# Performance work log

Measured on AMD Instinct MI355X. Metric: run time of the kernel, lower is better.

## Reference

```python
import jax, jax.numpy as jnp
import numpy as np

ALPHA = 0.25
GAMMA = 2.0
OBJ_POS_WEIGHT = 1.5
CLS_W, REG_W, OBJ_W = 2.5, 5.0, 0.5
B, M, C, IMG = 64, 50, 4, 1280


def setup_inputs() -> dict:
    key = jax.random.key(0)
    ks = jax.random.split(key, 12)
    shapes = {
        'cls_p3': (B, C, 160, 160), 'reg_p3': (B, 4, 160, 160), 'obj_p3': (B, 1, 160, 160),
        'cls_p4': (B, C, 80, 80),   'reg_p4': (B, 4, 80, 80),   'obj_p4': (B, 1, 80, 80),
        'cls_p5': (B, C, 40, 40),   'reg_p5': (B, 4, 40, 40),   'obj_p5': (B, 1, 40, 40),
    }
    inp = {name: jax.random.normal(k, s, dtype=jnp.float32)
           for (name, s), k in zip(shapes.items(), ks[:9])}
    # boxes in pixel xyxy: sample two corners uniformly, sort so x2>=x1, y2>=y1
    raw = jax.random.uniform(ks[9], (B, M, 4), dtype=jnp.float32) * IMG
    x1 = jnp.minimum(raw[..., 0], raw[..., 2]); x2 = jnp.maximum(raw[..., 0], raw[..., 2])
    y1 = jnp.minimum(raw[..., 1], raw[..., 3]); y2 = jnp.maximum(raw[..., 1], raw[..., 3])
    inp['boxes'] = jnp.stack([x1, y1, x2, y2], axis=-1)
    inp['labels'] = jax.random.randint(ks[10], (B, M), 0, C, dtype=jnp.int32)
    inp['box_valid'] = jax.random.randint(ks[11], (B, M), 0, 2, dtype=jnp.int32)
    inp['img_size'] = IMG
    return inp


def _bce_logits(x, t):
    # numerically stable BCE-with-logits, elementwise
    return jnp.maximum(x, 0.0) - x * t + jnp.log1p(jnp.exp(-jnp.abs(x)))


def _focal(x, t):
    bce = _bce_logits(x, t)
    p = jax.nn.sigmoid(x)
    p_t = p * t + (1.0 - p) * (1.0 - t)
    a_w = ALPHA * t + (1.0 - ALPHA) * (1.0 - t)
    return jnp.mean(a_w * (1.0 - p_t) ** GAMMA * bce)


def _smooth_l1(d):
    a = jnp.abs(d)
    return jnp.where(a < 1.0, 0.5 * d * d, a - 0.5)


def _build_targets(boxes, labels, valid, stride, Bn, Cn, H, W):
    cx = (boxes[..., 0] + boxes[..., 2]) * 0.5 / stride  # [B,M]
    cy = (boxes[..., 1] + boxes[..., 3]) * 0.5 / stride
    gx = jnp.clip(cx.astype(jnp.int32), 0, W - 1)
    gy = jnp.clip(cy.astype(jnp.int32), 0, H - 1)
    gy_s = jnp.where(valid > 0, gy, H)  # invalid boxes -> out of bounds -> dropped
    b = jnp.broadcast_to(jnp.arange(Bn)[:, None], gx.shape)
    w = jnp.maximum(boxes[..., 2] - boxes[..., 0], 1.0)
    h = jnp.maximum(boxes[..., 3] - boxes[..., 1], 1.0)
    vals = jnp.stack([cx - gx.astype(cx.dtype), cy - gy.astype(cy.dtype),
                      jnp.log(w / stride), jnp.log(h / stride)], axis=-1)  # [B,M,4]
    cls_t = jnp.zeros((Bn, Cn, H, W), jnp.float32).at[b, labels, gy_s, gx].set(1.0, mode='drop')
    obj_t = jnp.zeros((Bn, 1, H, W), jnp.float32).at[b, 0, gy_s, gx].set(1.0, mode='drop')
    ch = jnp.arange(4)
    reg_t = jnp.zeros((Bn, 4, H, W), jnp.float32).at[
        b[:, :, None], ch[None, None, :], gy_s[:, :, None], gx[:, :, None]].set(vals, mode='drop')
    mask = jnp.zeros((Bn, 1, H, W), jnp.float32).at[b, 0, gy_s, gx].set(1.0, mode='drop')
    return cls_t, reg_t, obj_t, mask


def _detection_loss(scales, boxes, labels, valid):
    total_cls = jnp.float32(0.0); total_reg = jnp.float32(0.0); total_obj = jnp.float32(0.0)
    for (cls_p, reg_p, obj_p, stride) in scales:
        Bn, Cn, H, W = cls_p.shape
        cls_t, reg_t, obj_t, mask = _build_targets(boxes, labels, valid, stride, Bn, Cn, H, W)
        total_cls = total_cls + _focal(cls_p, cls_t)
        # BCEWithLogits with pos_weight on positives, mean reduction
        obj_bce = -(OBJ_POS_WEIGHT * obj_t * jax.nn.log_sigmoid(obj_p)
                    + (1.0 - obj_t) * jax.nn.log_sigmoid(-obj_p))
        total_obj = total_obj + jnp.mean(obj_bce)
        mask4 = jnp.broadcast_to(mask, reg_p.shape)
        denom = jnp.sum(mask4)
        reg_l = jnp.sum(_smooth_l1(reg_p - reg_t) * mask4) / jnp.maximum(denom, 1.0)
        total_reg = total_reg + jnp.where(denom > 0, reg_l, 0.0)
    total = CLS_W * total_cls + REG_W * total_reg + OBJ_W * total_obj
    return total, total_cls, total_reg, total_obj


def reference(cls_p3, reg_p3, obj_p3, cls_p4, reg_p4, obj_p4, cls_p5, reg_p5, obj_p5,
              boxes, labels, box_valid, img_size):
    scales = [(cls_p3, reg_p3, obj_p3, 8.0),
              (cls_p4, reg_p4, obj_p4, 16.0),
              (cls_p5, reg_p5, obj_p5, 32.0)]
    return _detection_loss(scales, boxes, labels, box_valid)
```

## Files before the change

kernel.cpp:

```cpp
#include <hip/hip_runtime.h>
#include <math.h>

static constexpr int Bn = 64, Mn = 50, Cn = 4;
static constexpr int CORR_BLOCKS = 64;
static constexpr int DENSE_BLOCKS = 512;
static constexpr int TOTAL_BLOCKS = CORR_BLOCKS + DENSE_BLOCKS;

static constexpr int BASE_OFF = 12 * 64;

#define LOG2E 1.4426950408889634f
#define LN2   0.6931471805599453f

__device__ __forceinline__ float frcp (float x){ return __builtin_amdgcn_rcpf(x); }
__device__ __forceinline__ float fexp2(float x){ return __builtin_amdgcn_exp2f(x); }
__device__ __forceinline__ float flog2(float x){ return __builtin_amdgcn_logf(x); }

__device__ __forceinline__ float proc4(float4 v, float cf) {
  float s = 0.f;
  const float* px = &v.x;
#pragma unroll
  for (int k = 0; k < 4; ++k) {
    float x = px[k];
    float e   = fexp2(-LOG2E * fabsf(x));
    float ope = 1.f + e;
    float u   = frcp(ope);
    float sp  = fmaxf(x, 0.f) + LN2 * flog2(ope);
    float p   = (x >= 0.f) ? u : (1.f - u);
    float w   = fmaf(cf, fmaf(0.75f, p * p, -1.f), 1.f);
    s = fmaf(sp, w, s);
  }
  return s;
}

__device__ __forceinline__ float wave_reduce(float v) {
#pragma unroll
  for (int off = 32; off > 0; off >>= 1) v += __shfl_down(v, off, 64);
  return v;
}

__global__ __launch_bounds__(1024, 8) void main_kernel(
    const float* __restrict__ cls3, const float* __restrict__ reg3, const float* __restrict__ obj3,
    const float* __restrict__ cls4, const float* __restrict__ reg4, const float* __restrict__ obj4,
    const float* __restrict__ cls5, const float* __restrict__ reg5, const float* __restrict__ obj5,
    const float* __restrict__ boxes, const int* __restrict__ labels, const int* __restrict__ valid,
    float* __restrict__ ws) {
  if (blockIdx.x < CORR_BLOCKS) {
    __shared__ int s_cell[3][Mn];
    __shared__ int s_lab[Mn];
    __shared__ float cacc[12];

    const int b = blockIdx.x;
    const int tid = threadIdx.x;
    if (tid < 12) cacc[tid] = 0.f;

    const int s = tid / Mn;
    const int m = tid - s * Mn;

    float x1 = 0.f, y1 = 0.f, x2 = 0.f, y2 = 0.f;
    int lab = 0, val = 0;
    float cx = 0.f, cy = 0.f, strf = 8.f;
    int gx = 0, gy = 0, cell = -1, W = 160;

    if (tid < 150) {
      const float* bp = boxes + ((size_t)b * Mn + m) * 4;
      x1 = bp[0]; y1 = bp[1]; x2 = bp[2]; y2 = bp[3];
      lab = labels[b * Mn + m];
      val = valid[b * Mn + m];
      if (s == 0) s_lab[m] = lab;

      W = 160 >> s;
      strf = (float)(8 << s);
      if (val > 0) {
        float inv_s = frcp(strf);
        cx = (x1 + x2) * 0.5f * inv_s;
        cy = (y1 + y2) * 0.5f * inv_s;
        gx = min(max((int)cx, 0), W - 1);
        gy = min(max((int)cy, 0), W - 1);
        cell = gy * W + gx;
      }
      s_cell[s][m] = cell;
    }
    __syncthreads();

    if (tid < 150 && cell >= 0) {
      const float* clsP = (s == 0) ? cls3 : ((s == 1) ? cls4 : cls5);
      const float* regP = (s == 0) ? reg3 : ((s == 1) ? reg4 : reg5);
      const float* objP = (s == 0) ? obj3 : ((s == 1) ? obj4 : obj5);

      bool firstObj = true, lastReg = true, firstCls = true;
      for (int j = 0; j < Mn; ++j) {
        if (j == m) continue;
        if (s_cell[s][j] != cell) continue;
        if (j < m) {
          firstObj = false;
          if (s_lab[j] == lab) firstCls = false;
        } else {
          lastReg = false;
        }
      }
      size_t plane = (size_t)W * W;
      size_t pix = (size_t)gy * W + gx;

      if (firstObj) {
        float x = objP[(size_t)b * plane + pix];
        float e = fexp2(-LOG2E * fabsf(x));
        float sp = fmaxf(x, 0.f) + LN2 * flog2(1.f + e);
        float corr = 0.5f * sp - 1.5f * x;
        atomicAdd(&cacc[3 + s], corr);
        atomicAdd(&cacc[9 + s], 4.0f);
      }
      if (firstCls) {
        float x = clsP[((size_t)b * Cn + lab) * plane + pix];
        float e = fexp2(-LOG2E * fabsf(x));
        float ope = 1.f + e;
        float u = frcp(ope);
        float sp = fmaxf(x, 0.f) + LN2 * flog2(ope);
        float spn = sp - x;
        float p = (x >= 0.f) ? u : (1.f - u);
        float q = 1.f - p;
        float corr = 0.25f * q * q * spn - 0.75f * p * p * sp;
        atomicAdd(&cacc[0 + s], corr);
      }
      if (lastReg) {
        float w = fmaxf(x2 - x1, 1.f), h = fmaxf(y2 - y1, 1.f);
        float inv_s = frcp(strf);
        float t0 = cx - (float)gx, t1 = cy - (float)gy;
        float t2 = LN2 * flog2(w * inv_s), t3 = LN2 * flog2(h * inv_s);
        const float* rp = regP + (size_t)b * 4 * plane + pix;
        float sum = 0.f, d, a;
        d = rp[0]         - t0; a = fabsf(d); sum += (a < 1.f) ? 0.5f * d * d : a - 0.5f;
        d = rp[plane]     - t1; a = fabsf(d); sum += (a < 1.f) ? 0.5f * d * d : a - 0.5f;
        d = rp[2 * plane] - t2; a = fabsf(d); sum += (a < 1.f) ? 0.5f * d * d : a - 0.5f;
        d = rp[3 * plane] - t3; a = fabsf(d); sum += (a < 1.f) ? 0.5f * d * d : a - 0.5f;
        atomicAdd(&cacc[6 + s], sum);
      }
    }
    __syncthreads();
    if (tid < 12) ws[tid * 64 + b] = cacc[tid];
  } else {
    __shared__ float sdata[16];
    const int d = (int)blockIdx.x - CORR_BLOCKS;
    const int tid = threadIdx.x;

    const float4* sb; int bk, nB, nT; float cf;
    if (d < 311)      { sb = (const float4*)cls3; bk = d;       nB = 311; nT = 1600; cf = 1.f; }
    else if (d < 389) { sb = (const float4*)cls4; bk = d - 311; nB = 78;  nT = 400;  cf = 1.f; }
    else if (d < 409) { sb = (const float4*)cls5; bk = d - 389; nB = 20;  nT = 100;  cf = 1.f; }
    else if (d < 487) { sb = (const float4*)obj3; bk = d - 409; nB = 78;  nT = 400;  cf = 0.f; }
    else if (d < 507) { sb = (const float4*)obj4; bk = d - 487; nB = 20;  nT = 100;  cf = 0.f; }
    else              { sb = (const float4*)obj5; bk = d - 507; nB = 5;   nT = 25;   cf = 0.f; }

    float s = 0.f;
    int t = bk;
    float4 v = sb[(size_t)t * 1024 + tid];
    for (t += nB; t < nT; t += nB) {
      float4 vn = sb[(size_t)t * 1024 + tid];
      s += proc4(v, cf);
      v = vn;
    }
    s += proc4(v, cf);

    s = wave_reduce(s);
    const int lane = tid & 63;
    const int wid = tid >> 6;
    if (lane == 0) sdata[wid] = s;
    __syncthreads();
    if (tid == 0) {
      float r = 0.f;
#pragma unroll
      for (int i = 0; i < 16; ++i) r += sdata[i];
      ws[BASE_OFF + d] = r;
    }
  }
}

__global__ __launch_bounds__(256) void finalize_kernel(
    const float* __restrict__ ws, float* __restrict__ out) {
  __shared__ float sdata[6][4];
  __shared__ float res[18];
  const int t = threadIdx.x;
  const int lane = t & 63;
  const int wid = t >> 6;

  float a0 = 0.f, a1 = 0.f, a2 = 0.f, a3 = 0.f, a4 = 0.f, a5 = 0.f;
  for (int i = t; i < DENSE_BLOCKS; i += 256) {
    float v = ws[BASE_OFF + i];
    if (i < 311)      a0 += v;
    else if (i < 389) a1 += v;
    else if (i < 409) a2 += v;
    else if (i < 487) a3 += v;
    else if (i < 507) a4 += v;
    else              a5 += v;
  }
  float acc[6] = {a0, a1, a2, a3, a4, a5};
#pragma unroll
  for (int k = 0; k < 6; ++k) {
    float s = wave_reduce(acc[k]);
    if (lane == 0) sdata[k][wid] = s;
  }
  __syncthreads();
  if (t < 6) res[t] = sdata[t][0] + sdata[t][1] + sdata[t][2] + sdata[t][3];

  if (wid == 0) {
#pragma unroll
    for (int j = 0; j < 12; ++j) {
      float v = ws[j * 64 + lane];
      v = wave_reduce(v);
      if (lane == 0) res[6 + j] = v;
    }
  }
  __syncthreads();

  if (t == 0) {
    const float cls_cnt[3] = {6553600.f, 1638400.f, 409600.f};
    const float obj_cnt[3] = {1638400.f, 409600.f, 102400.f};
    float tc = 0.f, to = 0.f, tr = 0.f;
#pragma unroll
    for (int s = 0; s < 3; ++s) {
      tc += (res[s] + res[6 + s]) / cls_cnt[s];
      to += (res[3 + s] + res[9 + s]) / obj_cnt[s];
      float den = res[15 + s];
      if (den > 0.f) tr += res[12 + s] / fmaxf(den, 1.f);
    }
    float total = 2.5f * tc + 5.0f * tr + 0.5f * to;
    out[0] = total; out[1] = tc; out[2] = tr; out[3] = to;
  }
}

extern "C" void kernel_launch(void* const* d_in, const int* in_sizes, int n_in,
                              void* d_out, int out_size, void* d_ws, size_t ws_size,
                              hipStream_t stream) {
  const float* cls3 = (const float*)d_in[0];
  const float* reg3 = (const float*)d_in[1];
  const float* obj3 = (const float*)d_in[2];
  const float* cls4 = (const float*)d_in[3];
  const float* reg4 = (const float*)d_in[4];
  const float* obj4 = (const float*)d_in[5];
  const float* cls5 = (const float*)d_in[6];
  const float* reg5 = (const float*)d_in[7];
  const float* obj5 = (const float*)d_in[8];
  const float* boxes = (const float*)d_in[9];
  const int* labels = (const int*)d_in[10];
  const int* valid = (const int*)d_in[11];
  float* ws = (float*)d_ws;
  float* out = (float*)d_out;

  main_kernel<<<TOTAL_BLOCKS, 1024, 0, stream>>>(
      cls3, reg3, obj3, cls4, reg4, obj4, cls5, reg5, obj5,
      boxes, labels, valid, ws);

  finalize_kernel<<<1, 256, 0, stream>>>(ws, out);
}
```

Measured before the change: 22.94 us.

## Fuse correction work into dense blocks and issue fixed five-load chunks per block

The separate correction blocks are removed. Their box-matching work now runs inside the first 64 dense blocks, after those blocks have already issued their dense loads. Each dense block now handles exactly five float4 chunks per thread, loaded up front instead of through a strided loop, giving 525 evenly sized blocks. The goal is to hide load latency behind the correction work and to balance per-block load. The cost is higher register pressure and longer run times for the first 64 blocks.

```diff
diff --git a/kernel.cpp b/kernel.cpp
--- a/kernel.cpp
+++ b/kernel.cpp
@@ -2,9 +2,7 @@
 #include <math.h>
 
 static constexpr int Bn = 64, Mn = 50, Cn = 4;
-static constexpr int CORR_BLOCKS = 64;
-static constexpr int DENSE_BLOCKS = 512;
-static constexpr int TOTAL_BLOCKS = CORR_BLOCKS + DENSE_BLOCKS;
+static constexpr int TOTAL_BLOCKS = 525;
 
 static constexpr int BASE_OFF = 12 * 64;
 
@@ -44,13 +42,31 @@
     const float* __restrict__ cls5, const float* __restrict__ reg5, const float* __restrict__ obj5,
     const float* __restrict__ boxes, const int* __restrict__ labels, const int* __restrict__ valid,
     float* __restrict__ ws) {
-  if (blockIdx.x < CORR_BLOCKS) {
+  __shared__ float sdata[16];
+  const int bid = blockIdx.x;
+  const int tid = threadIdx.x;
+
+  const float4* sb; int lb; float cf;
+  if (bid < 320)      { sb = (const float4*)cls3; lb = bid;       cf = 1.f; }
+  else if (bid < 400) { sb = (const float4*)cls4; lb = bid - 320; cf = 1.f; }
+  else if (bid < 420) { sb = (const float4*)cls5; lb = bid - 400; cf = 1.f; }
+  else if (bid < 500) { sb = (const float4*)obj3; lb = bid - 420; cf = 0.f; }
+  else if (bid < 520) { sb = (const float4*)obj4; lb = bid - 500; cf = 0.f; }
+  else                { sb = (const float4*)obj5; lb = bid - 520; cf = 0.f; }
+
+  const float4* p = sb + (size_t)lb * 5120 + tid;
+  float4 v0 = p[0];
+  float4 v1 = p[1024];
+  float4 v2 = p[2048];
+  float4 v3 = p[3072];
+  float4 v4 = p[4096];
+
+  if (bid < 64) {
     __shared__ int s_cell[3][Mn];
     __shared__ int s_lab[Mn];
     __shared__ float cacc[12];
 
-    const int b = blockIdx.x;
-    const int tid = threadIdx.x;
+    const int b = bid;
     if (tid < 12) cacc[tid] = 0.f;
 
     const int s = tid / Mn;
@@ -116,9 +132,9 @@
         float u = frcp(ope);
         float sp = fmaxf(x, 0.f) + LN2 * flog2(ope);
         float spn = sp - x;
-        float p = (x >= 0.f) ? u : (1.f - u);
-        float q = 1.f - p;
-        float corr = 0.25f * q * q * spn - 0.75f * p * p * sp;
+        float p2 = (x >= 0.f) ? u : (1.f - u);
+        float q = 1.f - p2;
+        float corr = 0.25f * q * q * spn - 0.75f * p2 * p2 * sp;
         atomicAdd(&cacc[0 + s], corr);
       }
       if (lastReg) {
@@ -127,50 +143,31 @@
         float t0 = cx - (float)gx, t1 = cy - (float)gy;
         float t2 = LN2 * flog2(w * inv_s), t3 = LN2 * flog2(h * inv_s);
         const float* rp = regP + (size_t)b * 4 * plane + pix;
-        float sum = 0.f, d, a;
-        d = rp[0]         - t0; a = fabsf(d); sum += (a < 1.f) ? 0.5f * d * d : a - 0.5f;
-        d = rp[plane]     - t1; a = fabsf(d); sum += (a < 1.f) ? 0.5f * d * d : a - 0.5f;
-        d = rp[2 * plane] - t2; a = fabsf(d); sum += (a < 1.f) ? 0.5f * d * d : a - 0.5f;
-        d = rp[3 * plane] - t3; a = fabsf(d); sum += (a < 1.f) ? 0.5f * d * d : a - 0.5f;
+        float sum = 0.f, dd, a;
+        dd = rp[0]         - t0; a = fabsf(dd); sum += (a < 1.f) ? 0.5f * dd * dd : a - 0.5f;
+        dd = rp[plane]     - t1; a = fabsf(dd); sum += (a < 1.f) ? 0.5f * dd * dd : a - 0.5f;
+        dd = rp[2 * plane] - t2; a = fabsf(dd); sum += (a < 1.f) ? 0.5f * dd * dd : a - 0.5f;
+        dd = rp[3 * plane] - t3; a = fabsf(dd); sum += (a < 1.f) ? 0.5f * dd * dd : a - 0.5f;
         atomicAdd(&cacc[6 + s], sum);
       }
     }
     __syncthreads();
     if (tid < 12) ws[tid * 64 + b] = cacc[tid];
-  } else {
-    __shared__ float sdata[16];
-    const int d = (int)blockIdx.x - CORR_BLOCKS;
-    const int tid = threadIdx.x;
-
-    const float4* sb; int bk, nB, nT; float cf;
-    if (d < 311)      { sb = (const float4*)cls3; bk = d;       nB = 311; nT = 1600; cf = 1.f; }
-    else if (d < 389) { sb = (const float4*)cls4; bk = d - 311; nB = 78;  nT = 400;  cf = 1.f; }
-    else if (d < 409) { sb = (const float4*)cls5; bk = d - 389; nB = 20;  nT = 100;  cf = 1.f; }
-    else if (d < 487) { sb = (const float4*)obj3; bk = d - 409; nB = 78;  nT = 400;  cf = 0.f; }
-    else if (d < 507) { sb = (const float4*)obj4; bk = d - 487; nB = 20;  nT = 100;  cf = 0.f; }
-    else              { sb = (const float4*)obj5; bk = d - 507; nB = 5;   nT = 25;   cf = 0.f; }
-
-    float s = 0.f;
-    int t = bk;
-    float4 v = sb[(size_t)t * 1024 + tid];
-    for (t += nB; t < nT; t += nB) {
-      float4 vn = sb[(size_t)t * 1024 + tid];
-      s += proc4(v, cf);
-      v = vn;
-    }
-    s += proc4(v, cf);
-
-    s = wave_reduce(s);
-    const int lane = tid & 63;
-    const int wid = tid >> 6;
-    if (lane == 0) sdata[wid] = s;
-    __syncthreads();
-    if (tid == 0) {
-      float r = 0.f;
-#pragma unroll
-      for (int i = 0; i < 16; ++i) r += sdata[i];
-      ws[BASE_OFF + d] = r;
-    }
+  }
+
+  float s = proc4(v0, cf) + proc4(v1, cf) + proc4(v2, cf)
+          + proc4(v3, cf) + proc4(v4, cf);
+
+  s = wave_reduce(s);
+  const int lane = tid & 63;
+  const int wid = tid >> 6;
+  if (lane == 0) sdata[wid] = s;
+  __syncthreads();
+  if (tid == 0) {
+    float r = 0.f;
+#pragma unroll
+    for (int i = 0; i < 16; ++i) r += sdata[i];
+    ws[BASE_OFF + bid] = r;
   }
 }
 
@@ -183,13 +180,13 @@
   const int wid = t >> 6;
 
   float a0 = 0.f, a1 = 0.f, a2 = 0.f, a3 = 0.f, a4 = 0.f, a5 = 0.f;
-  for (int i = t; i < DENSE_BLOCKS; i += 256) {
+  for (int i = t; i < TOTAL_BLOCKS; i += 256) {
     float v = ws[BASE_OFF + i];
-    if (i < 311)      a0 += v;
-    else if (i < 389) a1 += v;
-    else if (i < 409) a2 += v;
-    else if (i < 487) a3 += v;
-    else if (i < 507) a4 += v;
+    if (i < 320)      a0 += v;
+    else if (i < 400) a1 += v;
+    else if (i < 420) a2 += v;
+    else if (i < 500) a3 += v;
+    else if (i < 520) a4 += v;
     else              a5 += v;
   }
   float acc[6] = {a0, a1, a2, a3, a4, a5};
```

Result: slower. 25.83 us (+12.6%).
